# Kernel tuning notes

Hardware: AMD Instinct MI355X
Metric: run time of the kernel (lower is better)

The kernel has to match this reference:

```python
import jax, jax.numpy as jnp
import numpy as np

N = 50000        # num nodes
D = 128          # hidden_dim
E = 800000       # num edges (avg_degree = 16)
LN_EPS = 1e-5    # torch LayerNorm default eps


def setup_inputs() -> dict:
    key = jax.random.key(0)
    ks = jax.random.split(key, 8)
    x = jax.random.normal(ks[0], (N, D), dtype=jnp.float32)
    edge_rows = jax.random.randint(ks[1], (E,), 0, N, dtype=jnp.int32)
    edge_cols = jax.random.randint(ks[2], (E,), 0, N, dtype=jnp.int32)
    # Parameters (xavier_uniform for lin1 gain=1.0, lin2 gain=0.5; zero biases)
    lim1 = float(np.sqrt(6.0 / (D + D)))           # gain 1.0
    lim2 = 0.5 * float(np.sqrt(6.0 / (D + D)))     # gain 0.5
    W1 = jax.random.uniform(ks[3], (D, D), minval=-lim1, maxval=lim1, dtype=jnp.float32)
    W2 = jax.random.uniform(ks[4], (D, D), minval=-lim2, maxval=lim2, dtype=jnp.float32)
    b1 = jnp.zeros((D,), dtype=jnp.float32)
    b2 = jnp.zeros((D,), dtype=jnp.float32)
    gamma = jnp.ones((D,), dtype=jnp.float32)      # LayerNorm weight
    beta = jnp.zeros((D,), dtype=jnp.float32)      # LayerNorm bias
    eps = jnp.zeros((), dtype=jnp.float32)         # learnable eps, init 0.0
    return {"x": x, "edge_rows": edge_rows, "edge_cols": edge_cols,
            "W1": W1, "b1": b1, "W2": W2, "b2": b2,
            "gamma": gamma, "beta": beta, "eps": eps}


def layer_norm(x, gamma, beta):
    mu = jnp.mean(x, axis=-1, keepdims=True)
    var = jnp.mean((x - mu) ** 2, axis=-1, keepdims=True)
    return (x - mu) * jax.lax.rsqrt(var + LN_EPS) * gamma + beta


def reference(x, edge_rows, edge_cols, W1, b1, W2, b2, gamma, beta, eps):
    h = layer_norm(x, gamma, beta)                               # [N, D]
    # sparse.mm(adj_t, h): neighbor_sum[i] = sum over edges (i <- j) of h[j]
    neighbor_sum = jax.ops.segment_sum(h[edge_cols], edge_rows, num_segments=N)
    h = (1.0 + eps) * h + neighbor_sum
    h = jax.nn.silu(h @ W1.T + b1)                               # lin1 + SiLU
    h = h @ W2.T + b2                                            # lin2 (dropout p=0 -> identity)
    return x + h
```

## Files before the change

### kernel.cpp

```cpp
#include <hip/hip_runtime.h>
#include <hip/hip_bf16.h>

#define N_NODES 50000
#define DIM 128
#define N_EDGES 800000
#define NBUCKETS 196
#define BINA_EPB 4096
#define NBLKA 196
#define SEGCAP 64
#define BUCKET_CAP 6144
#define LN_BLOCKS 12500
#define BSTRIDE_U32 16384

typedef __bf16 bf16_t;
typedef bf16_t bf16x2 __attribute__((ext_vector_type(2)));
typedef bf16_t bf16x4 __attribute__((ext_vector_type(4)));
typedef bf16_t bf16x8 __attribute__((ext_vector_type(8)));
typedef float f32x4 __attribute__((ext_vector_type(4)));

__device__ __forceinline__ float bf_lo(unsigned int u) {
  return __uint_as_float(u << 16);
}
__device__ __forceinline__ float bf_hi(unsigned int u) {
  return __uint_as_float(u & 0xffff0000u);
}

__global__ __launch_bounds__(256) void k_ln_binA(
    const float* __restrict__ x, const float* __restrict__ gamma,
    const float* __restrict__ beta, bf16_t* __restrict__ h,
    const int* __restrict__ erows, const int* __restrict__ ecols,
    unsigned int* __restrict__ tmp, int* __restrict__ cnt) {
  __shared__ int sh_hist[256];
  __shared__ int sh_cur[256];
  const int t = threadIdx.x;

  if (blockIdx.x < NBLKA) {
    const int blk = blockIdx.x;
    sh_hist[t] = 0;
    __syncthreads();
    const int base = blk * BINA_EPB;
    int bkt[16];
    unsigned int pk[16];
#pragma unroll
    for (int i = 0; i < 16; ++i) {
      const int e = base + i * 256 + t;
      if (e < N_EDGES) {
        const int d = erows[e];
        bkt[i] = d >> 8;
        pk[i] = ((unsigned int)(d & 255) << 16) | (unsigned int)ecols[e];
        atomicAdd(&sh_hist[bkt[i]], 1);
      } else {
        bkt[i] = -1;
      }
    }
    __syncthreads();
    if (t < NBUCKETS) cnt[t * NBLKA + blk] = min(sh_hist[t], SEGCAP);
    sh_cur[t] = 0;
    __syncthreads();
#pragma unroll
    for (int i = 0; i < 16; ++i) {
      if (bkt[i] >= 0) {
        const int pos = atomicAdd(&sh_cur[bkt[i]], 1);
        if (pos < SEGCAP)
          tmp[(size_t)bkt[i] * BSTRIDE_U32 + blk * SEGCAP + pos] = pk[i];
      }
    }
    return;
  }

  const int lane = t & 63;
  const int row  = (blockIdx.x - NBLKA) * 4 + (t >> 6);
  const float2 v = *(const float2*)(x + (size_t)row * DIM + lane * 2);
  float s  = v.x + v.y;
  float ss = v.x * v.x + v.y * v.y;
#pragma unroll
  for (int d = 1; d < 64; d <<= 1) {
    s  += __shfl_xor(s, d);
    ss += __shfl_xor(ss, d);
  }
  const float mu   = s * (1.0f / 128.0f);
  const float var  = ss * (1.0f / 128.0f) - mu * mu;
  const float rstd = rsqrtf(var + 1e-5f);
  const float2 g = *(const float2*)(gamma + lane * 2);
  const float2 b = *(const float2*)(beta + lane * 2);
  const float h0 = (v.x - mu) * rstd * g.x + b.x;
  const float h1 = (v.y - mu) * rstd * g.y + b.y;
  *(bf16x2*)(h + (size_t)row * DIM + lane * 2) = (bf16x2){(bf16_t)h0, (bf16_t)h1};
}

__global__ __launch_bounds__(1024) void k_binB_gather(
    const unsigned int* __restrict__ tmp, const int* __restrict__ cnt,
    const uint2* __restrict__ h4, const float* __restrict__ epsp,
    bf16_t* __restrict__ acc) {
  __shared__ unsigned int stage[BUCKET_CAP];
  __shared__ unsigned short sortedL[BUCKET_CAP];
  __shared__ int segoff[256];
  __shared__ int segcnt[256];
  __shared__ int sh_cnt[256];
  __shared__ int nst[256], nen[256];
  __shared__ int sh_cur[256];
  __shared__ int wsum[4];
  const int b = blockIdx.x, t = threadIdx.x;
  const int lane = t & 63, w = t >> 6;

  int c = 0, v = 0;
  if (t < 256) {
    c = (t < NBLKA) ? cnt[b * NBLKA + t] : 0;
    segcnt[t] = c;
    v = c;
#pragma unroll
    for (int d = 1; d < 64; d <<= 1) {
      const int n = __shfl_up(v, d);
      if (lane >= d) v += n;
    }
    if (lane == 63) wsum[w] = v;
  }
  __syncthreads();
  int total = wsum[0] + wsum[1] + wsum[2] + wsum[3];
  if (total > BUCKET_CAP) total = BUCKET_CAP;
  if (t < 256) {
    int woff = 0;
    for (int k = 0; k < w; ++k) woff += wsum[k];
    segoff[t] = v + woff - c;
    sh_cnt[t] = 0;
  }
  __syncthreads();

  {
    const int seg = t >> 2, sub = t & 3;
    if (seg < NBLKA) {
      const int cs = segcnt[seg], so = segoff[seg];
      const unsigned int* sp = tmp + (size_t)b * BSTRIDE_U32 + seg * SEGCAP;
      for (int j = sub; j < cs; j += 4)
        if (so + j < BUCKET_CAP) stage[so + j] = sp[j];
    }
  }
  __syncthreads();

  for (int e = t; e < total; e += 1024)
    atomicAdd(&sh_cnt[stage[e] >> 16], 1);
  __syncthreads();

  int val = 0, v2 = 0;
  if (t < 256) {
    val = sh_cnt[t];
    v2 = val;
#pragma unroll
    for (int d = 1; d < 64; d <<= 1) {
      const int n = __shfl_up(v2, d);
      if (lane >= d) v2 += n;
    }
    if (lane == 63) wsum[w] = v2;
  }
  __syncthreads();
  if (t < 256) {
    int woff = 0;
    for (int k = 0; k < w; ++k) woff += wsum[k];
    const int st = v2 + woff - val;
    nst[t] = st; nen[t] = st + val;
    sh_cur[t] = st;
  }
  __syncthreads();

  for (int e = t; e < total; e += 1024) {
    const unsigned int pv = stage[e];
    const int pos = atomicAdd(&sh_cur[pv >> 16], 1);
    sortedL[pos] = (unsigned short)(pv & 0xffffu);
  }
  __syncthreads();

  const int half = lane >> 5;
  const int l31  = lane & 31;
  const float epv = 1.0f + epsp[0];
  for (int n = w * 16; n < w * 16 + 16; ++n) {
    const int gnode = b * 256 + n;
    if (gnode >= N_NODES) continue;
    const int s = nst[n], e = nen[n];
    f32x4 a0 = {0.f, 0.f, 0.f, 0.f};
    f32x4 a1 = {0.f, 0.f, 0.f, 0.f};
    f32x4 a2 = {0.f, 0.f, 0.f, 0.f};
    f32x4 a3 = {0.f, 0.f, 0.f, 0.f};
    for (int base = s; base < e; base += 64) {
      const int cnt2 = e - base;
      const int m = cnt2 < 64 ? cnt2 : 64;
      const int myidx = (lane < m) ? (int)sortedL[base + lane] : 0;
      for (int j = 0; j < m; j += 8) {
        const int o0 = j + half;
        const int o1 = j + 2 + half;
        const int o2 = j + 4 + half;
        const int o3 = j + 6 + half;
        const int s0 = __shfl(myidx, o0);
        const int s1 = __shfl(myidx, o1);
        const int s2 = __shfl(myidx, o2);
        const int s3 = __shfl(myidx, o3);
        uint2 v0 = h4[(size_t)s0 * 32 + l31];
        uint2 v1 = h4[(size_t)s1 * 32 + l31];
        uint2 v2_ = h4[(size_t)s2 * 32 + l31];
        uint2 v3 = h4[(size_t)s3 * 32 + l31];
        if (o0 >= m) { v0.x = 0u; v0.y = 0u; }
        if (o1 >= m) { v1.x = 0u; v1.y = 0u; }
        if (o2 >= m) { v2_.x = 0u; v2_.y = 0u; }
        if (o3 >= m) { v3.x = 0u; v3.y = 0u; }
        a0[0] += bf_lo(v0.x); a0[1] += bf_hi(v0.x);
        a0[2] += bf_lo(v0.y); a0[3] += bf_hi(v0.y);
        a1[0] += bf_lo(v1.x); a1[1] += bf_hi(v1.x);
        a1[2] += bf_lo(v1.y); a1[3] += bf_hi(v1.y);
        a2[0] += bf_lo(v2_.x); a2[1] += bf_hi(v2_.x);
        a2[2] += bf_lo(v2_.y); a2[3] += bf_hi(v2_.y);
        a3[0] += bf_lo(v3.x); a3[1] += bf_hi(v3.x);
        a3[2] += bf_lo(v3.y); a3[3] += bf_hi(v3.y);
      }
    }
    f32x4 tt = (a0 + a1) + (a2 + a3);
#pragma unroll
    for (int k = 0; k < 4; ++k) tt[k] += __shfl_xor(tt[k], 32);
    if (half == 0) {
      const uint2 hv = h4[(size_t)gnode * 32 + l31];
      tt[0] += bf_lo(hv.x) * epv; tt[1] += bf_hi(hv.x) * epv;
      tt[2] += bf_lo(hv.y) * epv; tt[3] += bf_hi(hv.y) * epv;
      *(bf16x4*)(acc + (size_t)gnode * DIM + l31 * 4) =
          (bf16x4){(bf16_t)tt[0], (bf16_t)tt[1], (bf16_t)tt[2], (bf16_t)tt[3]};
    }
  }
}

__global__ __launch_bounds__(256) void k_mlp(
    const bf16_t* __restrict__ acc, const float* __restrict__ x,
    const float* __restrict__ W1, const float* __restrict__ b1,
    const float* __restrict__ W2, const float* __restrict__ b2,
    float* __restrict__ out) {
  __shared__ __attribute__((aligned(16))) bf16_t lsA[128 * 136];
  __shared__ __attribute__((aligned(16))) bf16_t lsB[128 * 136];

  const int tid  = threadIdx.x;
  const int lane = tid & 63;
  const int w    = tid >> 6;
  const int l15  = lane & 15;
  const int lq   = lane >> 4;

#pragma unroll
  for (int i = 0; i < 16; ++i) {
    const int idx = i * 1024 + tid * 4;
    const int r = idx >> 7, c = idx & 127;
    const float4 v1 = *(const float4*)(W1 + idx);
    const float4 v2 = *(const float4*)(W2 + idx);
    *(bf16x4*)&lsA[r * 136 + c] =
        (bf16x4){(bf16_t)v1.x, (bf16_t)v1.y, (bf16_t)v1.z, (bf16_t)v1.w};
    *(bf16x4*)&lsB[r * 136 + c] =
        (bf16x4){(bf16_t)v2.x, (bf16_t)v2.y, (bf16_t)v2.z, (bf16_t)v2.w};
  }

  const int rb = blockIdx.x * 128 + w * 32;

  bf16x8 af[2][4];
#pragma unroll
  for (int t = 0; t < 2; ++t)
#pragma unroll
    for (int ks = 0; ks < 4; ++ks) {
      int row = rb + t * 16 + l15;
      row = row < N_NODES ? row : N_NODES - 1;
      af[t][ks] = *(const bf16x8*)(acc + (size_t)row * DIM + ks * 32 + lq * 8);
    }
  __syncthreads();

  f32x4 c1[2][8] = {};
#pragma unroll
  for (int cb = 0; cb < 8; ++cb)
#pragma unroll
    for (int ks = 0; ks < 4; ++ks) {
      const bf16x8 bf = *(const bf16x8*)&lsA[(cb * 16 + l15) * 136 + ks * 32 + lq * 8];
      c1[0][cb] = __builtin_amdgcn_mfma_f32_16x16x32_bf16(af[0][ks], bf, c1[0][cb], 0, 0, 0);
      c1[1][cb] = __builtin_amdgcn_mfma_f32_16x16x32_bf16(af[1][ks], bf, c1[1][cb], 0, 0, 0);
    }
  __syncthreads();

#pragma unroll
  for (int cb = 0; cb < 8; ++cb) {
    const float b1v = b1[cb * 16 + l15];
#pragma unroll
    for (int t = 0; t < 2; ++t)
#pragma unroll
      for (int r = 0; r < 4; ++r) {
        float v = c1[t][cb][r] + b1v;
        v = v / (1.0f + __expf(-v));
        const int ri = w * 32 + t * 16 + lq * 4 + r;
        lsA[ri * 136 + cb * 16 + l15] = (bf16_t)v;
      }
  }
  __syncthreads();

  bf16x8 a2[2][4];
#pragma unroll
  for (int t = 0; t < 2; ++t)
#pragma unroll
    for (int ks = 0; ks < 4; ++ks)
      a2[t][ks] = *(const bf16x8*)&lsA[(w * 32 + t * 16 + l15) * 136 + ks * 32 + lq * 8];

  f32x4 c2[2][8] = {};
#pragma unroll
  for (int cb = 0; cb < 8; ++cb)
#pragma unroll
    for (int ks = 0; ks < 4; ++ks) {
      const bf16x8 bf = *(const bf16x8*)&lsB[(cb * 16 + l15) * 136 + ks * 32 + lq * 8];
      c2[0][cb] = __builtin_amdgcn_mfma_f32_16x16x32_bf16(a2[0][ks], bf, c2[0][cb], 0, 0, 0);
      c2[1][cb] = __builtin_amdgcn_mfma_f32_16x16x32_bf16(a2[1][ks], bf, c2[1][cb], 0, 0, 0);
    }

#pragma unroll
  for (int cb = 0; cb < 8; ++cb) {
    const int c = cb * 16 + l15;
    const float b2v = b2[c];
#pragma unroll
    for (int t = 0; t < 2; ++t)
#pragma unroll
      for (int r = 0; r < 4; ++r) {
        const int row = rb + t * 16 + lq * 4 + r;
        if (row < N_NODES)
          out[(size_t)row * DIM + c] = x[(size_t)row * DIM + c] + c2[t][cb][r] + b2v;
      }
  }
}

extern "C" void kernel_launch(void* const* d_in, const int* in_sizes, int n_in,
                              void* d_out, int out_size, void* d_ws, size_t ws_size,
                              hipStream_t stream) {
  const float* x     = (const float*)d_in[0];
  const int*   erows = (const int*)d_in[1];
  const int*   ecols = (const int*)d_in[2];
  const float* W1    = (const float*)d_in[3];
  const float* b1    = (const float*)d_in[4];
  const float* W2    = (const float*)d_in[5];
  const float* b2    = (const float*)d_in[6];
  const float* gamma = (const float*)d_in[7];
  const float* beta  = (const float*)d_in[8];
  const float* eps   = (const float*)d_in[9];
  float* out = (float*)d_out;

  char* ws = (char*)d_ws;
  bf16_t* h         = (bf16_t*)(ws);
  bf16_t* acc       = (bf16_t*)(ws + 12800000);
  unsigned int* tmp = (unsigned int*)(ws + 12800000);
  int*    cnt       = (int*)(ws + 25700000);

  k_ln_binA<<<LN_BLOCKS + NBLKA, 256, 0, stream>>>(x, gamma, beta, h,
                                                   erows, ecols, tmp, cnt);
  k_binB_gather<<<NBUCKETS, 1024, 0, stream>>>(tmp, cnt, (const uint2*)h, eps, acc);
  k_mlp<<<(N_NODES + 127) / 128, 256, 0, stream>>>(acc, x, W1, b1, W2, b2, out);
}
```

Before: 90.27 us.

## Fuse bucket sort, neighbor gather and MLP into one kernel per quarter-bucket

Merges the bucket-sort/gather kernel and the MLP kernel into one kernel, with four 256-thread blocks per bucket, each handling 64 nodes. Each block scans the bucket's edge segments twice with vector loads, counting and then placing only its own nodes' edges, which removes the shared staging copy. The aggregated rows stay in LDS and feed the MFMA MLP directly, so the bf16 acc round trip through global memory and one launch go away. In exchange, each block re-reads the whole bucket's edge list. Weights are now read from global and converted to bf16 inside the MFMA loops instead of being staged in LDS.

```diff
diff --git a/kernel.cpp b/kernel.cpp
--- a/kernel.cpp
+++ b/kernel.cpp
@@ -8,9 +8,9 @@
 #define BINA_EPB 4096
 #define NBLKA 196
 #define SEGCAP 64
-#define BUCKET_CAP 6144
+#define BSTRIDE_U32 16384
 #define LN_BLOCKS 12500
-#define BSTRIDE_U32 16384
+#define QCAP 2048
 
 typedef __bf16 bf16_t;
 typedef bf16_t bf16x2 __attribute__((ext_vector_type(2)));
@@ -88,84 +88,74 @@
   *(bf16x2*)(h + (size_t)row * DIM + lane * 2) = (bf16x2){(bf16_t)h0, (bf16_t)h1};
 }
 
-__global__ __launch_bounds__(1024) void k_binB_gather(
+__global__ __launch_bounds__(256) void k_bgm(
     const unsigned int* __restrict__ tmp, const int* __restrict__ cnt,
     const uint2* __restrict__ h4, const float* __restrict__ epsp,
-    bf16_t* __restrict__ acc) {
-  __shared__ unsigned int stage[BUCKET_CAP];
-  __shared__ unsigned short sortedL[BUCKET_CAP];
-  __shared__ int segoff[256];
-  __shared__ int segcnt[256];
-  __shared__ int sh_cnt[256];
-  __shared__ int nst[256], nen[256];
-  __shared__ int sh_cur[256];
-  __shared__ int wsum[4];
-  const int b = blockIdx.x, t = threadIdx.x;
-  const int lane = t & 63, w = t >> 6;
-
-  int c = 0, v = 0;
-  if (t < 256) {
-    c = (t < NBLKA) ? cnt[b * NBLKA + t] : 0;
-    segcnt[t] = c;
-    v = c;
+    const float* __restrict__ x,
+    const float* __restrict__ W1, const float* __restrict__ b1,
+    const float* __restrict__ W2, const float* __restrict__ b2,
+    float* __restrict__ out) {
+  __shared__ unsigned short sortedL[QCAP];
+  __shared__ __attribute__((aligned(16))) bf16_t accL[64 * 132];
+  __shared__ int nc[64], nstL[64], nenL[64], ncur[64];
+  const int b = blockIdx.x >> 2, q = blockIdx.x & 3;
+  const int t = threadIdx.x, lane = t & 63, w = t >> 6;
+  const int nlo = q * 64;
+
+  if (t < 64) nc[t] = 0;
+  __syncthreads();
+
+  if (t < NBLKA) {
+    const int cs = cnt[b * NBLKA + t];
+    const uint4* sp = (const uint4*)(tmp + (size_t)b * BSTRIDE_U32 + t * SEGCAP);
+    for (int j = 0; j < cs; j += 4) {
+      const uint4 e4 = sp[j >> 2];
+      const unsigned int ev[4] = {e4.x, e4.y, e4.z, e4.w};
+      const int rem = cs - j;
+#pragma unroll
+      for (int k = 0; k < 4; ++k) {
+        if (k < rem) {
+          const int d = (int)(ev[k] >> 16) - nlo;
+          if ((unsigned)d < 64u) atomicAdd(&nc[d], 1);
+        }
+      }
+    }
+  }
+  __syncthreads();
+
+  if (t < 64) {
+    const int val = nc[t];
+    int v = val;
 #pragma unroll
     for (int d = 1; d < 64; d <<= 1) {
       const int n = __shfl_up(v, d);
       if (lane >= d) v += n;
     }
-    if (lane == 63) wsum[w] = v;
+    const int st = v - val;
+    nstL[t] = st < QCAP ? st : QCAP;
+    nenL[t] = (st + val) < QCAP ? (st + val) : QCAP;
+    ncur[t] = st;
   }
   __syncthreads();
-  int total = wsum[0] + wsum[1] + wsum[2] + wsum[3];
-  if (total > BUCKET_CAP) total = BUCKET_CAP;
-  if (t < 256) {
-    int woff = 0;
-    for (int k = 0; k < w; ++k) woff += wsum[k];
-    segoff[t] = v + woff - c;
-    sh_cnt[t] = 0;
-  }
-  __syncthreads();
-
-  {
-    const int seg = t >> 2, sub = t & 3;
-    if (seg < NBLKA) {
-      const int cs = segcnt[seg], so = segoff[seg];
-      const unsigned int* sp = tmp + (size_t)b * BSTRIDE_U32 + seg * SEGCAP;
-      for (int j = sub; j < cs; j += 4)
-        if (so + j < BUCKET_CAP) stage[so + j] = sp[j];
-    }
-  }
-  __syncthreads();
-
-  for (int e = t; e < total; e += 1024)
-    atomicAdd(&sh_cnt[stage[e] >> 16], 1);
-  __syncthreads();
-
-  int val = 0, v2 = 0;
-  if (t < 256) {
-    val = sh_cnt[t];
-    v2 = val;
-#pragma unroll
-    for (int d = 1; d < 64; d <<= 1) {
-      const int n = __shfl_up(v2, d);
-      if (lane >= d) v2 += n;
-    }
-    if (lane == 63) wsum[w] = v2;
-  }
-  __syncthreads();
-  if (t < 256) {
-    int woff = 0;
-    for (int k = 0; k < w; ++k) woff += wsum[k];
-    const int st = v2 + woff - val;
-    nst[t] = st; nen[t] = st + val;
-    sh_cur[t] = st;
-  }
-  __syncthreads();
-
-  for (int e = t; e < total; e += 1024) {
-    const unsigned int pv = stage[e];
-    const int pos = atomicAdd(&sh_cur[pv >> 16], 1);
-    sortedL[pos] = (unsigned short)(pv & 0xffffu);
+
+  if (t < NBLKA) {
+    const int cs = cnt[b * NBLKA + t];
+    const uint4* sp = (const uint4*)(tmp + (size_t)b * BSTRIDE_U32 + t * SEGCAP);
+    for (int j = 0; j < cs; j += 4) {
+      const uint4 e4 = sp[j >> 2];
+      const unsigned int ev[4] = {e4.x, e4.y, e4.z, e4.w};
+      const int rem = cs - j;
+#pragma unroll
+      for (int k = 0; k < 4; ++k) {
+        if (k < rem) {
+          const int d = (int)(ev[k] >> 16) - nlo;
+          if ((unsigned)d < 64u) {
+            const int pos = atomicAdd(&ncur[d], 1);
+            if (pos < QCAP) sortedL[pos] = (unsigned short)(ev[k] & 0xffffu);
+          }
+        }
+      }
+    }
   }
   __syncthreads();
 
@@ -173,12 +163,16 @@
   const int l31  = lane & 31;
   const float epv = 1.0f + epsp[0];
   for (int n = w * 16; n < w * 16 + 16; ++n) {
-    const int gnode = b * 256 + n;
-    if (gnode >= N_NODES) continue;
-    const int s = nst[n], e = nen[n];
+    const int gnode = b * 256 + nlo + n;
+    if (gnode >= N_NODES) {
+      if (half == 0)
+        *(bf16x4*)&accL[n * 132 + l31 * 4] = (bf16x4){(bf16_t)0.f, (bf16_t)0.f, (bf16_t)0.f, (bf16_t)0.f};
+      continue;
+    }
+    const int s = nstL[n], e = nenL[n];
     f32x4 a0 = {0.f, 0.f, 0.f, 0.f};
     f32x4 a1 = {0.f, 0.f, 0.f, 0.f};
-    f32x4 a2 = {0.f, 0.f, 0.f, 0.f};
+    f32x4 a2v = {0.f, 0.f, 0.f, 0.f};
     f32x4 a3 = {0.f, 0.f, 0.f, 0.f};
     for (int base = s; base < e; base += 64) {
       const int cnt2 = e - base;
@@ -195,129 +189,97 @@
         const int s3 = __shfl(myidx, o3);
         uint2 v0 = h4[(size_t)s0 * 32 + l31];
         uint2 v1 = h4[(size_t)s1 * 32 + l31];
-        uint2 v2_ = h4[(size_t)s2 * 32 + l31];
+        uint2 v2 = h4[(size_t)s2 * 32 + l31];
         uint2 v3 = h4[(size_t)s3 * 32 + l31];
         if (o0 >= m) { v0.x = 0u; v0.y = 0u; }
         if (o1 >= m) { v1.x = 0u; v1.y = 0u; }
-        if (o2 >= m) { v2_.x = 0u; v2_.y = 0u; }
+        if (o2 >= m) { v2.x = 0u; v2.y = 0u; }
         if (o3 >= m) { v3.x = 0u; v3.y = 0u; }
         a0[0] += bf_lo(v0.x); a0[1] += bf_hi(v0.x);
         a0[2] += bf_lo(v0.y); a0[3] += bf_hi(v0.y);
         a1[0] += bf_lo(v1.x); a1[1] += bf_hi(v1.x);
         a1[2] += bf_lo(v1.y); a1[3] += bf_hi(v1.y);
-        a2[0] += bf_lo(v2_.x); a2[1] += bf_hi(v2_.x);
-        a2[2] += bf_lo(v2_.y); a2[3] += bf_hi(v2_.y);
+        a2v[0] += bf_lo(v2.x); a2v[1] += bf_hi(v2.x);
+        a2v[2] += bf_lo(v2.y); a2v[3] += bf_hi(v2.y);
         a3[0] += bf_lo(v3.x); a3[1] += bf_hi(v3.x);
         a3[2] += bf_lo(v3.y); a3[3] += bf_hi(v3.y);
       }
     }
-    f32x4 tt = (a0 + a1) + (a2 + a3);
+    f32x4 tt = (a0 + a1) + (a2v + a3);
 #pragma unroll
     for (int k = 0; k < 4; ++k) tt[k] += __shfl_xor(tt[k], 32);
     if (half == 0) {
       const uint2 hv = h4[(size_t)gnode * 32 + l31];
       tt[0] += bf_lo(hv.x) * epv; tt[1] += bf_hi(hv.x) * epv;
       tt[2] += bf_lo(hv.y) * epv; tt[3] += bf_hi(hv.y) * epv;
-      *(bf16x4*)(acc + (size_t)gnode * DIM + l31 * 4) =
+      *(bf16x4*)&accL[n * 132 + l31 * 4] =
           (bf16x4){(bf16_t)tt[0], (bf16_t)tt[1], (bf16_t)tt[2], (bf16_t)tt[3]};
     }
   }
-}
-
-__global__ __launch_bounds__(256) void k_mlp(
-    const bf16_t* __restrict__ acc, const float* __restrict__ x,
-    const float* __restrict__ W1, const float* __restrict__ b1,
-    const float* __restrict__ W2, const float* __restrict__ b2,
-    float* __restrict__ out) {
-  __shared__ __attribute__((aligned(16))) bf16_t lsA[128 * 136];
-  __shared__ __attribute__((aligned(16))) bf16_t lsB[128 * 136];
-
-  const int tid  = threadIdx.x;
-  const int lane = tid & 63;
-  const int w    = tid >> 6;
-  const int l15  = lane & 15;
-  const int lq   = lane >> 4;
-
-#pragma unroll
-  for (int i = 0; i < 16; ++i) {
-    const int idx = i * 1024 + tid * 4;
-    const int r = idx >> 7, c = idx & 127;
-    const float4 v1 = *(const float4*)(W1 + idx);
-    const float4 v2 = *(const float4*)(W2 + idx);
-    *(bf16x4*)&lsA[r * 136 + c] =
-        (bf16x4){(bf16_t)v1.x, (bf16_t)v1.y, (bf16_t)v1.z, (bf16_t)v1.w};
-    *(bf16x4*)&lsB[r * 136 + c] =
-        (bf16x4){(bf16_t)v2.x, (bf16_t)v2.y, (bf16_t)v2.z, (bf16_t)v2.w};
-  }
-
-  const int rb = blockIdx.x * 128 + w * 32;
-
-  bf16x8 af[2][4];
-#pragma unroll
-  for (int t = 0; t < 2; ++t)
+
+  const int l15 = lane & 15;
+  const int lq  = lane >> 4;
+
+  bf16x8 af[4];
+#pragma unroll
+  for (int ks = 0; ks < 4; ++ks)
+    af[ks] = *(const bf16x8*)&accL[(w * 16 + l15) * 132 + ks * 32 + lq * 8];
+
+  f32x4 c1[8] = {};
+#pragma unroll
+  for (int cb = 0; cb < 8; ++cb) {
+    const float* wrow = W1 + (size_t)(cb * 16 + l15) * DIM;
 #pragma unroll
     for (int ks = 0; ks < 4; ++ks) {
-      int row = rb + t * 16 + l15;
-      row = row < N_NODES ? row : N_NODES - 1;
-      af[t][ks] = *(const bf16x8*)(acc + (size_t)row * DIM + ks * 32 + lq * 8);
-    }
-  __syncthreads();
-
-  f32x4 c1[2][8] = {};
-#pragma unroll
-  for (int cb = 0; cb < 8; ++cb)
-#pragma unroll
-    for (int ks = 0; ks < 4; ++ks) {
-      const bf16x8 bf = *(const bf16x8*)&lsA[(cb * 16 + l15) * 136 + ks * 32 + lq * 8];
-      c1[0][cb] = __builtin_amdgcn_mfma_f32_16x16x32_bf16(af[0][ks], bf, c1[0][cb], 0, 0, 0);
-      c1[1][cb] = __builtin_amdgcn_mfma_f32_16x16x32_bf16(af[1][ks], bf, c1[1][cb], 0, 0, 0);
-    }
-  __syncthreads();
+      const float4 u0 = *(const float4*)(wrow + ks * 32 + lq * 8);
+      const float4 u1 = *(const float4*)(wrow + ks * 32 + lq * 8 + 4);
+      const bf16x8 bf = (bf16x8){(bf16_t)u0.x, (bf16_t)u0.y, (bf16_t)u0.z, (bf16_t)u0.w,
+                                 (bf16_t)u1.x, (bf16_t)u1.y, (bf16_t)u1.z, (bf16_t)u1.w};
+      c1[cb] = __builtin_amdgcn_mfma_f32_16x16x32_bf16(af[ks], bf, c1[cb], 0, 0, 0);
+    }
+  }
 
 #pragma unroll
   for (int cb = 0; cb < 8; ++cb) {
     const float b1v = b1[cb * 16 + l15];
 #pragma unroll
-    for (int t = 0; t < 2; ++t)
-#pragma unroll
-      for (int r = 0; r < 4; ++r) {
-        float v = c1[t][cb][r] + b1v;
-        v = v / (1.0f + __expf(-v));
-        const int ri = w * 32 + t * 16 + lq * 4 + r;
-        lsA[ri * 136 + cb * 16 + l15] = (bf16_t)v;
-      }
-  }
-  __syncthreads();
-
-  bf16x8 a2[2][4];
-#pragma unroll
-  for (int t = 0; t < 2; ++t)
-#pragma unroll
-    for (int ks = 0; ks < 4; ++ks)
-      a2[t][ks] = *(const bf16x8*)&lsA[(w * 32 + t * 16 + l15) * 136 + ks * 32 + lq * 8];
-
-  f32x4 c2[2][8] = {};
-#pragma unroll
-  for (int cb = 0; cb < 8; ++cb)
+    for (int r = 0; r < 4; ++r) {
+      float v = c1[cb][r] + b1v;
+      v = v / (1.0f + __expf(-v));
+      accL[(w * 16 + lq * 4 + r) * 132 + cb * 16 + l15] = (bf16_t)v;
+    }
+  }
+
+  bf16x8 a2[4];
+#pragma unroll
+  for (int ks = 0; ks < 4; ++ks)
+    a2[ks] = *(const bf16x8*)&accL[(w * 16 + l15) * 132 + ks * 32 + lq * 8];
+
+  f32x4 c2[8] = {};
+#pragma unroll
+  for (int cb = 0; cb < 8; ++cb) {
+    const float* wrow = W2 + (size_t)(cb * 16 + l15) * DIM;
 #pragma unroll
     for (int ks = 0; ks < 4; ++ks) {
-      const bf16x8 bf = *(const bf16x8*)&lsB[(cb * 16 + l15) * 136 + ks * 32 + lq * 8];
-      c2[0][cb] = __builtin_amdgcn_mfma_f32_16x16x32_bf16(a2[0][ks], bf, c2[0][cb], 0, 0, 0);
-      c2[1][cb] = __builtin_amdgcn_mfma_f32_16x16x32_bf16(a2[1][ks], bf, c2[1][cb], 0, 0, 0);
-    }
-
+      const float4 u0 = *(const float4*)(wrow + ks * 32 + lq * 8);
+      const float4 u1 = *(const float4*)(wrow + ks * 32 + lq * 8 + 4);
+      const bf16x8 bf = (bf16x8){(bf16_t)u0.x, (bf16_t)u0.y, (bf16_t)u0.z, (bf16_t)u0.w,
+                                 (bf16_t)u1.x, (bf16_t)u1.y, (bf16_t)u1.z, (bf16_t)u1.w};
+      c2[cb] = __builtin_amdgcn_mfma_f32_16x16x32_bf16(a2[ks], bf, c2[cb], 0, 0, 0);
+    }
+  }
+
+  const int rowbase = b * 256 + nlo + w * 16 + lq * 4;
 #pragma unroll
   for (int cb = 0; cb < 8; ++cb) {
     const int c = cb * 16 + l15;
     const float b2v = b2[c];
 #pragma unroll
-    for (int t = 0; t < 2; ++t)
-#pragma unroll
-      for (int r = 0; r < 4; ++r) {
-        const int row = rb + t * 16 + lq * 4 + r;
-        if (row < N_NODES)
-          out[(size_t)row * DIM + c] = x[(size_t)row * DIM + c] + c2[t][cb][r] + b2v;
-      }
+    for (int r = 0; r < 4; ++r) {
+      const int row = rowbase + r;
+      if (row < N_NODES)
+        out[(size_t)row * DIM + c] = x[(size_t)row * DIM + c] + c2[cb][r] + b2v;
+    }
   }
 }
 
@@ -338,12 +300,11 @@
 
   char* ws = (char*)d_ws;
   bf16_t* h         = (bf16_t*)(ws);
-  bf16_t* acc       = (bf16_t*)(ws + 12800000);
   unsigned int* tmp = (unsigned int*)(ws + 12800000);
-  int*    cnt       = (int*)(ws + 25700000);
+  int*    cnt       = (int*)(ws + 25645056);
 
   k_ln_binA<<<LN_BLOCKS + NBLKA, 256, 0, stream>>>(x, gamma, beta, h,
                                                    erows, ecols, tmp, cnt);
-  k_binB_gather<<<NBUCKETS, 1024, 0, stream>>>(tmp, cnt, (const uint2*)h, eps, acc);
-  k_mlp<<<(N_NODES + 127) / 128, 256, 0, stream>>>(acc, x, W1, b1, W2, b2, out);
-}
+  k_bgm<<<NBUCKETS * 4, 256, 0, stream>>>(tmp, cnt, (const uint2*)h, eps,
+                                          x, W1, b1, W2, b2, out);
+}
```

Measured after the change: 163.6 us. +81.2%, slower.
